# Kernel tuning notes

Hardware: AMD Instinct MI355X
Metric: run time of the kernel (lower is better)

The kernel has to match this reference:

```python
import jax, jax.numpy as jnp
from jax import lax
import numpy as np

B, N, T, F = 2, 100, 15, 6
K, H = 4, 128          # edge_types, n_hid
E = N * (N - 1)        # fully connected off-diagonal graph


def setup_inputs() -> dict:
    key = jax.random.key(0)
    ks = jax.random.split(key, 24)
    s = 0.1
    data = jax.random.normal(ks[0], (B, N, T, F), jnp.float32)
    rel_type = jax.random.uniform(ks[1], (B, E, K), jnp.float32)
    off = ~np.eye(N, dtype=bool)
    recv_idx, send_idx = np.where(off)
    eye = np.eye(N, dtype=np.float32)
    rel_rec = jnp.asarray(eye[recv_idx])    # [E, N]
    rel_send = jnp.asarray(eye[send_idx])   # [E, N]
    inp = {
        'data': data, 'rel_type': rel_type,
        'rel_rec': rel_rec, 'rel_send': rel_send,
        'pred_steps': 1,
        # message MLPs, stacked over edge types (weights stored [in, out])
        'W1': jax.random.normal(ks[2], (K, 2 * H, H), jnp.float32) * s,
        'b1': jax.random.normal(ks[3], (K, H), jnp.float32) * s,
        'W2': jax.random.normal(ks[4], (K, H, H), jnp.float32) * s,
        'b2': jax.random.normal(ks[5], (K, H), jnp.float32) * s,
        # GRU-style gates (hidden_* have no bias in the torch module)
        'Whr': jax.random.normal(ks[6], (H, H), jnp.float32) * s,
        'Whi': jax.random.normal(ks[7], (H, H), jnp.float32) * s,
        'Whh': jax.random.normal(ks[8], (H, H), jnp.float32) * s,
        'Wir': jax.random.normal(ks[9], (F, H), jnp.float32) * s,
        'bir': jax.random.normal(ks[10], (H,), jnp.float32) * s,
        'Wii': jax.random.normal(ks[11], (F, H), jnp.float32) * s,
        'bii': jax.random.normal(ks[12], (H,), jnp.float32) * s,
        'Win': jax.random.normal(ks[13], (F, H), jnp.float32) * s,
        'bin_': jax.random.normal(ks[14], (H,), jnp.float32) * s,
        # output MLP
        'Wo1': jax.random.normal(ks[15], (H, H), jnp.float32) * s,
        'bo1': jax.random.normal(ks[16], (H,), jnp.float32) * s,
        'Wo2': jax.random.normal(ks[17], (H, H), jnp.float32) * s,
        'bo2': jax.random.normal(ks[18], (H,), jnp.float32) * s,
        'Wo3': jax.random.normal(ks[19], (H, F), jnp.float32) * s,
        'bo3': jax.random.normal(ks[20], (F,), jnp.float32) * s,
    }
    return inp


def _forward(data, rel_type, rel_rec, rel_send, pred_steps,
             W1, b1, W2, b2, Whr, Whi, Whh,
             Wir, bir, Wii, bii, Win, bin_,
             Wo1, bo1, Wo2, bo2, Wo3, bo3):
    inputs = jnp.swapaxes(data, 1, 2)            # [B, T, N, F]
    Bn, Tn, Nn, Fn = inputs.shape
    norm = jnp.asarray(W1.shape[0], inputs.dtype)  # edge_types (skip_first=False)
    hidden0 = jnp.zeros((Bn, Nn, Whr.shape[0]), inputs.dtype)

    def step_fn(carry, xs):
        hidden, prev_pred = carry
        gt, step = xs
        ins = jnp.where(step % pred_steps == 0, gt, prev_pred)  # [B, N, F]
        recv = jnp.einsum('en,bnh->beh', rel_rec, hidden)
        send = jnp.einsum('en,bnh->beh', rel_send, hidden)
        pre_msg = jnp.concatenate([send, recv], axis=-1)        # [B, E, 2H]
        # all edge-type message MLPs fused into batched einsums
        m1 = jnp.tanh(jnp.einsum('bei,kih->bekh', pre_msg, W1) + b1)
        m2 = jnp.tanh(jnp.einsum('bekh,khj->bekj', m1, W2) + b2)
        all_msgs = jnp.einsum('bekh,bek->beh', m2, rel_type) / norm
        # aggregate messages onto receiving nodes; torch divides by inputs.size(2)=F
        agg = jnp.einsum('beh,en->bnh', all_msgs, rel_rec) / Fn  # [B, N, H]
        r = jax.nn.sigmoid(ins @ Wir + bir + agg @ Whr)
        i = jax.nn.sigmoid(ins @ Wii + bii + agg @ Whi)
        n = jnp.tanh(ins @ Win + bin_ + r * (agg @ Whh))
        hidden_new = (1.0 - i) * n + i * hidden
        p = jax.nn.relu(hidden_new @ Wo1 + bo1)
        p = jax.nn.relu(p @ Wo2 + bo2)
        pred = ins + (p @ Wo3 + bo3)
        return (hidden_new, pred), pred

    xs = (jnp.swapaxes(inputs[:, :-1], 0, 1), jnp.arange(Tn - 1))
    (_, _), preds = lax.scan(step_fn, (hidden0, inputs[:, 0]), xs)
    preds = jnp.swapaxes(preds, 0, 1)   # [B, T-1, N, F]
    return jnp.swapaxes(preds, 1, 2)    # [B, N, T-1, F]


def reference(data, rel_type, rel_rec, rel_send, pred_steps,
              W1, b1, W2, b2, Whr, Whi, Whh,
              Wir, bir, Wii, bii, Win, bin_,
              Wo1, bo1, Wo2, bo2, Wo3, bo3):
    return _forward(data, rel_type, rel_rec, rel_send, pred_steps,
                    W1, b1, W2, b2, Whr, Whi, Whh,
                    Wir, bir, Wii, bii, Win, bin_,
                    Wo1, bo1, Wo2, bo2, Wo3, bo3)
```

## Files before the change

kernel.cpp:

```cpp
#include <hip/hip_runtime.h>
#include <math.h>

#define BB 2
#define NN 100
#define TT 15
#define FF 6
#define KK 4
#define HH 128
#define EE 9900
#define EPN 99
#define NSTEP 14
#define TILE_E 64

__device__ __forceinline__ float fast_tanh(float x) {
    float e = __expf(2.0f * x);
    return 1.0f - __fdividef(2.0f, 1.0f + e);
}
__device__ __forceinline__ float fast_sig(float x) {
    return __fdividef(1.0f, 1.0f + __expf(-x));
}

__global__ __launch_bounds__(256) void k_init(
    const float* __restrict__ b1,
    float* __restrict__ hidden,
    float* __restrict__ agg4,
    float* __restrict__ Hs,
    float* __restrict__ Hr)
{
    int i = blockIdx.x * 256 + threadIdx.x;
    if (i < BB * NN * HH) hidden[i] = 0.f;
    agg4[i] = 0.f;
    int k  = (i >> 7) & 3;
    int hh = i & 127;
    Hs[i] = 0.f;
    Hr[i] = b1[k * HH + hh];
}

__global__ __launch_bounds__(256) void k_edge(
    const float* __restrict__ Hs,
    const float* __restrict__ Hr,
    const float* __restrict__ W2,
    const float* __restrict__ b2,
    const float* __restrict__ rel_type,
    float* __restrict__ agg4)
{
    const int tile = blockIdx.x;
    const int b    = blockIdx.y;
    const int k    = blockIdx.z;
    const int e0   = tile * TILE_E;
    const int t    = threadIdx.x;
    const int hg   = t & 15;
    const int eg   = t >> 4;
    const int h0   = hg * 8;

    __shared__ __align__(16) float m1[TILE_E][132];
    __shared__ __align__(16) float w2c[32][132];
    __shared__ int s_send[TILE_E], s_recv[TILE_E];

    if (t < TILE_E) {
        int e = e0 + t;
        if (e >= EE) e = EE - 1;
        int r = e / EPN;
        int j = e - r * EPN;
        s_recv[t] = r;
        s_send[t] = j + (j >= r ? 1 : 0);
    }
    __syncthreads();

    const float4* Hs4 = (const float4*)Hs;
    const float4* Hr4 = (const float4*)Hr;
#pragma unroll
    for (int rep = 0; rep < 8; ++rep) {
        int idx = rep * 256 + t;
        int el  = idx >> 5;
        int f4  = idx & 31;
        int s   = s_send[el];
        int r   = s_recv[el];
        float4 a = Hs4[((b * NN + s) * KK + k) * 32 + f4];
        float4 c = Hr4[((b * NN + r) * KK + k) * 32 + f4];
        float4 v;
        v.x = fast_tanh(a.x + c.x);
        v.y = fast_tanh(a.y + c.y);
        v.z = fast_tanh(a.z + c.z);
        v.w = fast_tanh(a.w + c.w);
        *(float4*)&m1[el][f4 * 4] = v;
    }

    int   el[4], erecv[4];
    float relw[4];
    const float scale = 1.0f / (KK * FF);
#pragma unroll
    for (int ei = 0; ei < 4; ++ei) {
        int l = eg + 16 * ei;
        el[ei] = l;
        int e = e0 + l;
        bool valid = (e < EE);
        if (!valid) e = EE - 1;
        erecv[ei] = s_recv[l];
        relw[ei]  = valid ? rel_type[(b * EE + e) * KK + k] * scale : 0.f;
    }

    const float4* W2f4 = (const float4*)(W2 + k * HH * HH);

    float acc[4][8] = {};
    for (int jc = 0; jc < 4; ++jc) {
        __syncthreads();
#pragma unroll
        for (int rep = 0; rep < 4; ++rep) {
            int s   = rep * 256 + t;
            int row = s >> 5;
            int c4  = s & 31;
            *(float4*)&w2c[row][c4 * 4] = W2f4[(jc * 32 + row) * 32 + c4];
        }
        __syncthreads();
#pragma unroll
        for (int js = 0; js < 8; ++js) {
            float4 wA[4], wB[4];
#pragma unroll
            for (int jj = 0; jj < 4; ++jj) {
                wA[jj] = *(const float4*)&w2c[js * 4 + jj][h0];
                wB[jj] = *(const float4*)&w2c[js * 4 + jj][h0 + 4];
            }
#pragma unroll
            for (int ei = 0; ei < 4; ++ei) {
                float4 mv = *(const float4*)&m1[el[ei]][jc * 32 + js * 4];
                float* A = acc[ei];
                A[0] = fmaf(mv.x, wA[0].x, fmaf(mv.y, wA[1].x, fmaf(mv.z, wA[2].x, fmaf(mv.w, wA[3].x, A[0]))));
                A[1] = fmaf(mv.x, wA[0].y, fmaf(mv.y, wA[1].y, fmaf(mv.z, wA[2].y, fmaf(mv.w, wA[3].y, A[1]))));
                A[2] = fmaf(mv.x, wA[0].z, fmaf(mv.y, wA[1].z, fmaf(mv.z, wA[2].z, fmaf(mv.w, wA[3].z, A[2]))));
                A[3] = fmaf(mv.x, wA[0].w, fmaf(mv.y, wA[1].w, fmaf(mv.z, wA[2].w, fmaf(mv.w, wA[3].w, A[3]))));
                A[4] = fmaf(mv.x, wB[0].x, fmaf(mv.y, wB[1].x, fmaf(mv.z, wB[2].x, fmaf(mv.w, wB[3].x, A[4]))));
                A[5] = fmaf(mv.x, wB[0].y, fmaf(mv.y, wB[1].y, fmaf(mv.z, wB[2].y, fmaf(mv.w, wB[3].y, A[5]))));
                A[6] = fmaf(mv.x, wB[0].z, fmaf(mv.y, wB[1].z, fmaf(mv.z, wB[2].z, fmaf(mv.w, wB[3].z, A[6]))));
                A[7] = fmaf(mv.x, wB[0].w, fmaf(mv.y, wB[1].w, fmaf(mv.z, wB[2].w, fmaf(mv.w, wB[3].w, A[7]))));
            }
        }
    }

    float b2k[8];
    *(float4*)&b2k[0] = *(const float4*)&b2[k * HH + h0];
    *(float4*)&b2k[4] = *(const float4*)&b2[k * HH + h0 + 4];

    const int rA = s_recv[0];
    const int rB = s_recv[TILE_E - 1];
    float sumA[8] = {}, sumB[8] = {};
#pragma unroll
    for (int ei = 0; ei < 4; ++ei) {
        bool isA = (erecv[ei] == rA);
#pragma unroll
        for (int h = 0; h < 8; ++h) {
            float v = relw[ei] * fast_tanh(acc[ei][h] + b2k[h]);
            if (isA) sumA[h] += v; else sumB[h] += v;
        }
    }

    float* red  = &m1[0][0];
    float* aggk = agg4 + ((size_t)(k * BB + b)) * NN * HH;
    __syncthreads();
    *(float4*)&red[eg * 128 + h0]     = make_float4(sumA[0], sumA[1], sumA[2], sumA[3]);
    *(float4*)&red[eg * 128 + h0 + 4] = make_float4(sumA[4], sumA[5], sumA[6], sumA[7]);
    __syncthreads();
    if (t < HH) {
        float s = 0.f;
#pragma unroll
        for (int y = 0; y < 16; ++y) s += red[y * 128 + t];
        atomicAdd(&aggk[rA * HH + t], s);
    }
    if (rB != rA) {
        __syncthreads();
        *(float4*)&red[eg * 128 + h0]     = make_float4(sumB[0], sumB[1], sumB[2], sumB[3]);
        *(float4*)&red[eg * 128 + h0 + 4] = make_float4(sumB[4], sumB[5], sumB[6], sumB[7]);
        __syncthreads();
        if (t < HH) {
            float s = 0.f;
#pragma unroll
            for (int y = 0; y < 16; ++y) s += red[y * 128 + t];
            atomicAdd(&aggk[rB * HH + t], s);
        }
    }
}

__global__ __launch_bounds__(256) void k_gru_out(
    const float* __restrict__ data,
    float* __restrict__ agg4,
    float* __restrict__ hidden,
    const float* __restrict__ W1,  const float* __restrict__ b1,
    const float* __restrict__ Whr, const float* __restrict__ Whi,
    const float* __restrict__ Whh,
    const float* __restrict__ Wir, const float* __restrict__ bir,
    const float* __restrict__ Wii, const float* __restrict__ bii,
    const float* __restrict__ Win, const float* __restrict__ bin_,
    const float* __restrict__ Wo1, const float* __restrict__ bo1,
    const float* __restrict__ Wo2, const float* __restrict__ bo2,
    const float* __restrict__ Wo3, const float* __restrict__ bo3,
    float* __restrict__ Hs,
    float* __restrict__ Hr,
    float* __restrict__ out,
    const int* __restrict__ ps_ptr, int step)
{
    const int bn = blockIdx.x;
    const int t  = threadIdx.x;
    const int tt = t & 127;
    const int jh = t >> 7;

    __shared__ float sa[HH], sh[HH], p1b[HH], p2b[HH], insb[8];
    __shared__ float gbuf[6][HH];
    __shared__ float mbuf[2][HH];

    if (t < HH) {
        float s = 0.f;
#pragma unroll
        for (int k = 0; k < KK; ++k) {
            size_t idx = ((size_t)k * BB * NN + bn) * HH + t;
            s += agg4[idx];
            agg4[idx] = 0.f;
        }
        sa[t] = s;
    }
    if (t < FF) {
        int ps = ps_ptr[0];
        bool use_gt = (ps <= 1) || (step % ps == 0);
        int prev = (step > 0) ? (step - 1) : 0;
        float gt = data[(bn * TT + step) * FF + t];
        float pv = out[(bn * NSTEP + prev) * FF + t];
        insb[t] = use_gt ? gt : pv;
    }
    __syncthreads();

    {
        float pr = 0.f, pi = 0.f, ph = 0.f;
        const int j0 = jh * 64;
#pragma unroll 4
        for (int jj = 0; jj < 64; ++jj) {
            int j = j0 + jj;
            float a = sa[j];
            pr = fmaf(a, Whr[j * HH + tt], pr);
            pi = fmaf(a, Whi[j * HH + tt], pi);
            ph = fmaf(a, Whh[j * HH + tt], ph);
        }
        gbuf[jh][tt] = pr; gbuf[2 + jh][tt] = pi; gbuf[4 + jh][tt] = ph;
    }
    __syncthreads();

    if (t < HH) {
        float ar = gbuf[0][t] + gbuf[1][t];
        float ai = gbuf[2][t] + gbuf[3][t];
        float ah = gbuf[4][t] + gbuf[5][t];
        float xr = bir[t], xi = bii[t], xn = bin_[t];
#pragma unroll
        for (int f = 0; f < FF; ++f) {
            float v = insb[f];
            xr = fmaf(v, Wir[f * HH + t], xr);
            xi = fmaf(v, Wii[f * HH + t], xi);
            xn = fmaf(v, Win[f * HH + t], xn);
        }
        float r  = fast_sig(xr + ar);
        float i  = fast_sig(xi + ai);
        float n  = fast_tanh(xn + r * ah);
        float hnew = (1.f - i) * n + i * hidden[bn * HH + t];
        hidden[bn * HH + t] = hnew;
        sh[t] = hnew;
    }
    __syncthreads();

    {
        float a1 = 0.f;
        const int j0 = jh * 64;
#pragma unroll 4
        for (int jj = 0; jj < 64; ++jj) { int j = j0 + jj; a1 = fmaf(sh[j], Wo1[j * HH + tt], a1); }
        mbuf[jh][tt] = a1;
    }
    __syncthreads();
    if (t < HH) p1b[t] = fmaxf(mbuf[0][t] + mbuf[1][t] + bo1[t], 0.f);
    __syncthreads();
    {
        float a2 = 0.f;
        const int j0 = jh * 64;
#pragma unroll 4
        for (int jj = 0; jj < 64; ++jj) { int j = j0 + jj; a2 = fmaf(p1b[j], Wo2[j * HH + tt], a2); }
        mbuf[jh][tt] = a2;
    }
    __syncthreads();
    if (t < HH) p2b[t] = fmaxf(mbuf[0][t] + mbuf[1][t] + bo2[t], 0.f);
    __syncthreads();

    if (t < FF) {
        float o = bo3[t];
#pragma unroll 4
        for (int j = 0; j < HH; ++j) o = fmaf(p2b[j], Wo3[j * FF + t], o);
        out[(bn * NSTEP + step) * FF + t] = insb[t] + o;
    }

    float pacc[4] = {0.f, 0.f, 0.f, 0.f};
    int pbase[4];
#pragma unroll
    for (int p = 0; p < 4; ++p) {
        int rep   = 2 * p + jh;
        int plane = 2 * (rep & 3) + (rep >> 2);
        pbase[p]  = plane * HH * HH + tt;
    }
#pragma unroll 2
    for (int j = 0; j < HH; ++j) {
        float hj = sh[j];
#pragma unroll
        for (int p = 0; p < 4; ++p)
            pacc[p] = fmaf(hj, W1[pbase[p] + j * HH], pacc[p]);
    }
#pragma unroll
    for (int p = 0; p < 4; ++p) {
        int rep = 2 * p + jh;
        int kk = rep & 3, which = rep >> 2;
        if (which == 0) Hs[(bn * KK + kk) * HH + tt] = pacc[p];
        else            Hr[(bn * KK + kk) * HH + tt] = pacc[p] + b1[kk * HH + tt];
    }
}

extern "C" void kernel_launch(void* const* d_in, const int* in_sizes, int n_in,
                              void* d_out, int out_size, void* d_ws, size_t ws_size,
                              hipStream_t stream) {
    const float* data     = (const float*)d_in[0];
    const float* rel_type = (const float*)d_in[1];
    const int*   ps_ptr   = (const int*)d_in[4];
    const float* W1   = (const float*)d_in[5];
    const float* b1   = (const float*)d_in[6];
    const float* W2   = (const float*)d_in[7];
    const float* b2   = (const float*)d_in[8];
    const float* Whr  = (const float*)d_in[9];
    const float* Whi  = (const float*)d_in[10];
    const float* Whh  = (const float*)d_in[11];
    const float* Wir  = (const float*)d_in[12];
    const float* bir  = (const float*)d_in[13];
    const float* Wii  = (const float*)d_in[14];
    const float* bii  = (const float*)d_in[15];
    const float* Win  = (const float*)d_in[16];
    const float* bin_ = (const float*)d_in[17];
    const float* Wo1  = (const float*)d_in[18];
    const float* bo1  = (const float*)d_in[19];
    const float* Wo2  = (const float*)d_in[20];
    const float* bo2  = (const float*)d_in[21];
    const float* Wo3  = (const float*)d_in[22];
    const float* bo3  = (const float*)d_in[23];

    float* out = (float*)d_out;

    float* ws     = (float*)d_ws;
    float* hidden = ws;
    float* Hs     = ws + 25600;
    float* Hr     = ws + 128000;
    float* agg4   = ws + 230400;

    k_init<<<400, 256, 0, stream>>>(b1, hidden, agg4, Hs, Hr);

    const int ntile = (EE + TILE_E - 1) / TILE_E;
    dim3 egrid(ntile, BB, KK);

    for (int step = 0; step < NSTEP; ++step) {
        k_edge<<<egrid, 256, 0, stream>>>(Hs, Hr, W2, b2, rel_type, agg4);
        k_gru_out<<<BB * NN, 256, 0, stream>>>(data, agg4, hidden,
                                               W1, b1,
                                               Whr, Whi, Whh,
                                               Wir, bir, Wii, bii, Win, bin_,
                                               Wo1, bo1, Wo2, bo2, Wo3, bo3,
                                               Hs, Hr, out, ps_ptr, step);
    }
}
```

Measured before the change: 1.122 ms.

## Widen GRU kernel to 512 threads and split edge columns across halves

The per-node GRU/output kernel goes from 256 to 512 threads. Each matvec's reduction dimension is split four ways with partial sums reduced in shared memory, and the W1 projection is split into half-plane chunks. This raises parallelism and memory-level concurrency in the latency-bound per-step kernel, at the cost of extra shared memory and reduction work. In the edge kernel each thread now owns two separate float4 column groups (cA, cB) instead of eight contiguous columns, to change the LDS access pattern for bank conflicts.

```diff
diff --git a/kernel.cpp b/kernel.cpp
--- a/kernel.cpp
+++ b/kernel.cpp
@@ -51,7 +51,8 @@
     const int t    = threadIdx.x;
     const int hg   = t & 15;
     const int eg   = t >> 4;
-    const int h0   = hg * 8;
+    const int cA   = hg * 4;
+    const int cB   = 64 + hg * 4;
 
     __shared__ __align__(16) float m1[TILE_E][132];
     __shared__ __align__(16) float w2c[32][132];
@@ -118,8 +119,8 @@
             float4 wA[4], wB[4];
 #pragma unroll
             for (int jj = 0; jj < 4; ++jj) {
-                wA[jj] = *(const float4*)&w2c[js * 4 + jj][h0];
-                wB[jj] = *(const float4*)&w2c[js * 4 + jj][h0 + 4];
+                wA[jj] = *(const float4*)&w2c[js * 4 + jj][cA];
+                wB[jj] = *(const float4*)&w2c[js * 4 + jj][cB];
             }
 #pragma unroll
             for (int ei = 0; ei < 4; ++ei) {
@@ -138,8 +139,8 @@
     }
 
     float b2k[8];
-    *(float4*)&b2k[0] = *(const float4*)&b2[k * HH + h0];
-    *(float4*)&b2k[4] = *(const float4*)&b2[k * HH + h0 + 4];
+    *(float4*)&b2k[0] = *(const float4*)&b2[k * HH + cA];
+    *(float4*)&b2k[4] = *(const float4*)&b2[k * HH + cB];
 
     const int rA = s_recv[0];
     const int rB = s_recv[TILE_E - 1];
@@ -157,8 +158,8 @@
     float* red  = &m1[0][0];
     float* aggk = agg4 + ((size_t)(k * BB + b)) * NN * HH;
     __syncthreads();
-    *(float4*)&red[eg * 128 + h0]     = make_float4(sumA[0], sumA[1], sumA[2], sumA[3]);
-    *(float4*)&red[eg * 128 + h0 + 4] = make_float4(sumA[4], sumA[5], sumA[6], sumA[7]);
+    *(float4*)&red[eg * 128 + cA] = make_float4(sumA[0], sumA[1], sumA[2], sumA[3]);
+    *(float4*)&red[eg * 128 + cB] = make_float4(sumA[4], sumA[5], sumA[6], sumA[7]);
     __syncthreads();
     if (t < HH) {
         float s = 0.f;
@@ -168,8 +169,8 @@
     }
     if (rB != rA) {
         __syncthreads();
-        *(float4*)&red[eg * 128 + h0]     = make_float4(sumB[0], sumB[1], sumB[2], sumB[3]);
-        *(float4*)&red[eg * 128 + h0 + 4] = make_float4(sumB[4], sumB[5], sumB[6], sumB[7]);
+        *(float4*)&red[eg * 128 + cA] = make_float4(sumB[0], sumB[1], sumB[2], sumB[3]);
+        *(float4*)&red[eg * 128 + cB] = make_float4(sumB[4], sumB[5], sumB[6], sumB[7]);
         __syncthreads();
         if (t < HH) {
             float s = 0.f;
@@ -180,7 +181,7 @@
     }
 }
 
-__global__ __launch_bounds__(256) void k_gru_out(
+__global__ __launch_bounds__(512) void k_gru_out(
     const float* __restrict__ data,
     float* __restrict__ agg4,
     float* __restrict__ hidden,
@@ -201,21 +202,18 @@
     const int bn = blockIdx.x;
     const int t  = threadIdx.x;
     const int tt = t & 127;
-    const int jh = t >> 7;
+    const int q  = t >> 7;
 
     __shared__ float sa[HH], sh[HH], p1b[HH], p2b[HH], insb[8];
-    __shared__ float gbuf[6][HH];
-    __shared__ float mbuf[2][HH];
-
-    if (t < HH) {
-        float s = 0.f;
-#pragma unroll
-        for (int k = 0; k < KK; ++k) {
-            size_t idx = ((size_t)k * BB * NN + bn) * HH + t;
-            s += agg4[idx];
-            agg4[idx] = 0.f;
-        }
-        sa[t] = s;
+    __shared__ float ap[4][HH];
+    __shared__ float gp[3][4][HH];
+    __shared__ float mp[4][HH];
+    __shared__ float pp[16][HH];
+
+    {
+        size_t idx = ((size_t)q * BB * NN + bn) * HH + tt;
+        ap[q][tt] = agg4[idx];
+        agg4[idx] = 0.f;
     }
     if (t < FF) {
         int ps = ps_ptr[0];
@@ -226,26 +224,28 @@
         insb[t] = use_gt ? gt : pv;
     }
     __syncthreads();
-
-    {
+    if (t < HH) sa[t] = ap[0][t] + ap[1][t] + ap[2][t] + ap[3][t];
+    __syncthreads();
+
+    {
+        const int j0 = q * 32;
         float pr = 0.f, pi = 0.f, ph = 0.f;
-        const int j0 = jh * 64;
-#pragma unroll 4
-        for (int jj = 0; jj < 64; ++jj) {
+#pragma unroll 8
+        for (int jj = 0; jj < 32; ++jj) {
             int j = j0 + jj;
             float a = sa[j];
             pr = fmaf(a, Whr[j * HH + tt], pr);
             pi = fmaf(a, Whi[j * HH + tt], pi);
             ph = fmaf(a, Whh[j * HH + tt], ph);
         }
-        gbuf[jh][tt] = pr; gbuf[2 + jh][tt] = pi; gbuf[4 + jh][tt] = ph;
+        gp[0][q][tt] = pr; gp[1][q][tt] = pi; gp[2][q][tt] = ph;
     }
     __syncthreads();
 
     if (t < HH) {
-        float ar = gbuf[0][t] + gbuf[1][t];
-        float ai = gbuf[2][t] + gbuf[3][t];
-        float ah = gbuf[4][t] + gbuf[5][t];
+        float ar = gp[0][0][t] + gp[0][1][t] + gp[0][2][t] + gp[0][3][t];
+        float ai = gp[1][0][t] + gp[1][1][t] + gp[1][2][t] + gp[1][3][t];
+        float ah = gp[2][0][t] + gp[2][1][t] + gp[2][2][t] + gp[2][3][t];
         float xr = bir[t], xi = bii[t], xn = bin_[t];
 #pragma unroll
         for (int f = 0; f < FF; ++f) {
@@ -264,24 +264,24 @@
     __syncthreads();
 
     {
+        const int j0 = q * 32;
         float a1 = 0.f;
-        const int j0 = jh * 64;
-#pragma unroll 4
-        for (int jj = 0; jj < 64; ++jj) { int j = j0 + jj; a1 = fmaf(sh[j], Wo1[j * HH + tt], a1); }
-        mbuf[jh][tt] = a1;
-    }
-    __syncthreads();
-    if (t < HH) p1b[t] = fmaxf(mbuf[0][t] + mbuf[1][t] + bo1[t], 0.f);
-    __syncthreads();
-    {
+#pragma unroll 8
+        for (int jj = 0; jj < 32; ++jj) { int j = j0 + jj; a1 = fmaf(sh[j], Wo1[j * HH + tt], a1); }
+        mp[q][tt] = a1;
+    }
+    __syncthreads();
+    if (t < HH) p1b[t] = fmaxf(mp[0][t] + mp[1][t] + mp[2][t] + mp[3][t] + bo1[t], 0.f);
+    __syncthreads();
+    {
+        const int j0 = q * 32;
         float a2 = 0.f;
-        const int j0 = jh * 64;
-#pragma unroll 4
-        for (int jj = 0; jj < 64; ++jj) { int j = j0 + jj; a2 = fmaf(p1b[j], Wo2[j * HH + tt], a2); }
-        mbuf[jh][tt] = a2;
-    }
-    __syncthreads();
-    if (t < HH) p2b[t] = fmaxf(mbuf[0][t] + mbuf[1][t] + bo2[t], 0.f);
+#pragma unroll 8
+        for (int jj = 0; jj < 32; ++jj) { int j = j0 + jj; a2 = fmaf(p1b[j], Wo2[j * HH + tt], a2); }
+        mp[q][tt] = a2;
+    }
+    __syncthreads();
+    if (t < HH) p2b[t] = fmaxf(mp[0][t] + mp[1][t] + mp[2][t] + mp[3][t] + bo2[t], 0.f);
     __syncthreads();
 
     if (t < FF) {
@@ -291,27 +291,31 @@
         out[(bn * NSTEP + step) * FF + t] = insb[t] + o;
     }
 
-    float pacc[4] = {0.f, 0.f, 0.f, 0.f};
-    int pbase[4];
-#pragma unroll
-    for (int p = 0; p < 4; ++p) {
-        int rep   = 2 * p + jh;
-        int plane = 2 * (rep & 3) + (rep >> 2);
-        pbase[p]  = plane * HH * HH + tt;
-    }
-#pragma unroll 2
-    for (int j = 0; j < HH; ++j) {
-        float hj = sh[j];
-#pragma unroll
-        for (int p = 0; p < 4; ++p)
-            pacc[p] = fmaf(hj, W1[pbase[p] + j * HH], pacc[p]);
-    }
-#pragma unroll
-    for (int p = 0; p < 4; ++p) {
-        int rep = 2 * p + jh;
-        int kk = rep & 3, which = rep >> 2;
-        if (which == 0) Hs[(bn * KK + kk) * HH + tt] = pacc[p];
-        else            Hr[(bn * KK + kk) * HH + tt] = pacc[p] + b1[kk * HH + tt];
+    {
+#pragma unroll
+        for (int i = 0; i < 4; ++i) {
+            int c     = 4 * q + i;
+            int plane = c >> 1;
+            int half  = c & 1;
+            const float* Wp = W1 + (size_t)plane * HH * HH + tt;
+            const int j0 = half * 64;
+            float acc = 0.f;
+#pragma unroll 8
+            for (int jj = 0; jj < 64; ++jj) {
+                int j = j0 + jj;
+                acc = fmaf(sh[j], Wp[j * HH], acc);
+            }
+            pp[c][tt] = acc;
+        }
+    }
+    __syncthreads();
+    for (int o = t; o < 1024; o += 512) {
+        int plane = o >> 7;
+        int col   = o & 127;
+        float v = pp[plane * 2][col] + pp[plane * 2 + 1][col];
+        int kk = plane >> 1, which = plane & 1;
+        if (which == 0) Hs[(bn * KK + kk) * HH + col] = v;
+        else            Hr[(bn * KK + kk) * HH + col] = v + b1[kk * HH + col];
     }
 }
 
@@ -356,7 +360,7 @@
 
     for (int step = 0; step < NSTEP; ++step) {
         k_edge<<<egrid, 256, 0, stream>>>(Hs, Hr, W2, b2, rel_type, agg4);
-        k_gru_out<<<BB * NN, 256, 0, stream>>>(data, agg4, hidden,
+        k_gru_out<<<BB * NN, 512, 0, stream>>>(data, agg4, hidden,
                                                W1, b1,
                                                Whr, Whi, Whh,
                                                Wir, bir, Wii, bii, Win, bin_,
```

Result: faster. 968.9 us (-13.6%).
